# Optimization experiments

Measured on AMD Instinct MI355X. Metric: run time of the kernel, lower is better.

The kernel has to match this reference:

```python
import jax, jax.numpy as jnp
import numpy as np

B, N1, N2, D, H = 32, 512, 256, 256, 8
HD = D // H  # head dim = 32


def setup_inputs() -> dict:
    key = jax.random.key(0)
    ks = jax.random.split(key, 12)
    s = 0.05
    return {
        "x1": jax.random.normal(ks[0], (B, N1, D), jnp.float32),
        "x2": jax.random.normal(ks[1], (B, N2, D), jnp.float32),
        "r_w1": jax.random.normal(ks[2], (D, 2 * D), jnp.float32) * s,
        "r_b1": jnp.zeros((D,), jnp.float32),
        "ln_g": jnp.ones((D,), jnp.float32),
        "ln_b": jnp.zeros((D,), jnp.float32),
        "r_w2": jax.random.normal(ks[3], (4, D), jnp.float32) * s,
        "r_b2": jnp.zeros((4,), jnp.float32),
        "lf_w": jax.random.normal(ks[4], (D, D), jnp.float32) * s,
        "lf_b": jnp.zeros((D,), jnp.float32),
        "af2_w": jax.random.normal(ks[5], (D, D), jnp.float32) * s,
        "af2_b": jnp.zeros((D,), jnp.float32),
        "af3_w": jax.random.normal(ks[6], (N1, D), jnp.float32) * s,  # Linear(dim, num_pathway)
        "af3_b": jnp.zeros((N1,), jnp.float32),
        "attn_in_w": jax.random.normal(ks[7], (3 * D, D), jnp.float32) * s,
        "attn_in_b": jnp.zeros((3 * D,), jnp.float32),
        "attn_out_w": jax.random.normal(ks[8], (D, D), jnp.float32) * s,
        "attn_out_b": jnp.zeros((D,), jnp.float32),
    }


def _layernorm(x, g, b, eps=1e-5):
    mu = x.mean(-1, keepdims=True)
    var = ((x - mu) ** 2).mean(-1, keepdims=True)
    return (x - mu) * jax.lax.rsqrt(var + eps) * g + b


def reference(x1, x2, r_w1, r_b1, ln_g, ln_b, r_w2, r_b2,
              lf_w, lf_b, af2_w, af2_b, af3_w, af3_b,
              attn_in_w, attn_in_b, attn_out_w, attn_out_b):
    b, n1, d = x1.shape
    n2 = x2.shape[1]

    # ---- RoutingNetwork: mean-pool both modalities, small MLP, softmax ----
    m = jnp.concatenate([x1.mean(1), x2.mean(1)], axis=-1)        # [b, 2d]
    h = jax.nn.gelu(_layernorm(m @ r_w1.T + r_b1, ln_g, ln_b), approximate=False)
    logits = h @ r_w2.T + r_b2                                     # [b, 4]
    w = jax.nn.softmax(logits, axis=-1)                            # [b, 4]

    z = jnp.concatenate([x1, x2], axis=1)                          # [b, n1+n2, d]

    # ---- Expert 0: LinearFusion (dropout off at eval) ----
    lf = jax.nn.elu(z @ lf_w.T + lf_b)
    g0, i0 = lf[:, :n1, :], lf[:, n1:, :]

    # ---- Expert 1: AddFusion, n1 >= n2 branch (n2 == dim required) ----
    a1 = jax.nn.elu(x1 @ af2_w.T + af2_b)                          # [b, n1, d]
    a2 = jax.nn.elu(jnp.einsum('bnd,pn->bdp', x2, af3_w) + af3_b)  # [b, d, n1]
    a2 = a2.transpose(0, 2, 1)                                     # [b, n1, d]
    x_out = a1 + a2
    g1, i1 = x_out, x_out[:, :n2, :]

    # ---- Expert 2: AttentionFusion (MHA, 8 heads, self-attn over concat) ----
    qkv = z @ attn_in_w.T + attn_in_b                              # [b, S, 3d]
    q, k, v = jnp.split(qkv, 3, axis=-1)
    S = n1 + n2
    q = q.reshape(b, S, H, HD)
    k = k.reshape(b, S, H, HD)
    v = v.reshape(b, S, H, HD)
    scores = jnp.einsum('bqhd,bkhd->bhqk', q, k) / np.sqrt(HD)
    attn = jax.nn.softmax(scores, axis=-1)
    o = jnp.einsum('bhqk,bkhd->bqhd', attn, v).reshape(b, S, d)
    o = o @ attn_out_w.T + attn_out_b
    g2, i2 = o[:, :n1, :], o[:, n1:, :]

    # ---- Expert 3: IdentityFusion ----
    g3, i3 = x1, x2

    # ---- Soft-routing weighted combine ----
    gene_all = jnp.stack([g0, g1, g2, g3], axis=1)                 # [b, 4, n1, d]
    img_all = jnp.stack([i0, i1, i2, i3], axis=1)                  # [b, 4, n2, d]
    we = w[:, :, None, None]
    gene = (gene_all * we).sum(axis=1)
    img = (img_all * we).sum(axis=1)
    return gene, img
```

## Files before the change

### kernel.cpp

```cpp
#include <hip/hip_runtime.h>
#include <hip/hip_bf16.h>
#include <math.h>

#define B_ 32
#define N1_ 512
#define N2_ 256
#define D_ 256
#define S_ 768
#define IMG_OFF 4194304
#define SCALE_ 0.17677669529663689f
#define QSCALE_ (0.17677669529663689f * 1.4426950408889634f)

typedef __attribute__((ext_vector_type(8))) short bf16x8;
typedef __attribute__((ext_vector_type(4))) float f32x4;
#define MFMA16(a, b, c) __builtin_amdgcn_mfma_f32_16x16x32_bf16(a, b, c, 0, 0, 0)

__device__ __forceinline__ ushort f2b(float f) {
  __hip_bfloat16 h = __float2bfloat16(f);
  return __builtin_bit_cast(ushort, h);
}
__device__ __forceinline__ float eluf(float v) { return v > 0.f ? v : expm1f(v); }

__global__ __launch_bounds__(256) void k_prep(const float* __restrict__ x1,
                                              const float* __restrict__ x2,
                                              ushort* __restrict__ zb,
                                              float* __restrict__ mp) {
  int b = blockIdx.x >> 3, s = blockIdx.x & 7;
  int t = threadIdx.x;
  int c = t & 63;
  int rg = t >> 6;
  __shared__ float red[4][260];
  float4 s1 = {0.f, 0.f, 0.f, 0.f};
  for (int i = 0; i < 16; ++i) {
    int r = s*64 + rg*16 + i;
    float4 v = *(const float4*)(x1 + ((size_t)(b*N1_) + r)*D_ + c*4);
    s1.x += v.x; s1.y += v.y; s1.z += v.z; s1.w += v.w;
    uint2 pk;
    pk.x = (uint)f2b(v.x) | ((uint)f2b(v.y) << 16);
    pk.y = (uint)f2b(v.z) | ((uint)f2b(v.w) << 16);
    *(uint2*)(zb + (size_t)b*196608 + (size_t)r*256 + c*4) = pk;
  }
  red[rg][c*4+0] = s1.x; red[rg][c*4+1] = s1.y; red[rg][c*4+2] = s1.z; red[rg][c*4+3] = s1.w;
  __syncthreads();
  {
    float v = red[0][t] + red[1][t] + red[2][t] + red[3][t];
    mp[(size_t)(b*8+s)*512 + t] = v * (1.0f/512.0f);
  }
  __syncthreads();
  float4 s2 = {0.f, 0.f, 0.f, 0.f};
  for (int i = 0; i < 8; ++i) {
    int r = s*32 + rg*8 + i;
    float4 v = *(const float4*)(x2 + ((size_t)(b*N2_) + r)*D_ + c*4);
    s2.x += v.x; s2.y += v.y; s2.z += v.z; s2.w += v.w;
    uint2 pk;
    pk.x = (uint)f2b(v.x) | ((uint)f2b(v.y) << 16);
    pk.y = (uint)f2b(v.z) | ((uint)f2b(v.w) << 16);
    *(uint2*)(zb + (size_t)b*196608 + (size_t)(512 + r)*256 + c*4) = pk;
  }
  red[rg][c*4+0] = s2.x; red[rg][c*4+1] = s2.y; red[rg][c*4+2] = s2.z; red[rg][c*4+3] = s2.w;
  __syncthreads();
  {
    float v = red[0][t] + red[1][t] + red[2][t] + red[3][t];
    mp[(size_t)(b*8+s)*512 + 256 + t] = v * (1.0f/256.0f);
  }
}

__global__ __launch_bounds__(256) void k_wcvt(const float* __restrict__ lf_w,
                                              const float* __restrict__ af2_w,
                                              const float* __restrict__ af3_w,
                                              const float* __restrict__ attn_in_w,
                                              const float* __restrict__ attn_out_w,
                                              ushort* __restrict__ wb) {
  int g = blockIdx.x*256 + threadIdx.x;
  int e0 = g*4;
  const float* src; int loc; float sc = 1.f;
  if (e0 < 65536)       { src = lf_w;       loc = e0; }
  else if (e0 < 131072) { src = af2_w;      loc = e0 - 65536; }
  else if (e0 < 262144) { src = af3_w;      loc = e0 - 131072; }
  else if (e0 < 458752) { src = attn_in_w;  loc = e0 - 262144; if (loc < 65536) sc = QSCALE_; }
  else                  { src = attn_out_w; loc = e0 - 458752; }
  float4 v = *(const float4*)(src + loc);
  *(ushort4*)(wb + e0) = make_ushort4(f2b(v.x*sc), f2b(v.y*sc), f2b(v.z*sc), f2b(v.w*sc));
}

__global__ __launch_bounds__(256) void k_head(const float* __restrict__ mp, const float* __restrict__ r_w1,
                       const float* __restrict__ r_b1, const float* __restrict__ ln_g,
                       const float* __restrict__ ln_b, const float* __restrict__ r_w2,
                       const float* __restrict__ r_b2, float* __restrict__ wout) {
  int b = blockIdx.x;
  int j = threadIdx.x;
  __shared__ float ms[512];
  __shared__ float red[256];
  float a0 = 0.f, a1 = 0.f;
  for (int s = 0; s < 8; ++s) {
    a0 += mp[(size_t)(b*8+s)*512 + j];
    a1 += mp[(size_t)(b*8+s)*512 + 256 + j];
  }
  ms[j] = a0; ms[j+256] = a1;
  __syncthreads();
  float acc = r_b1[j];
  const float* wrow = r_w1 + (size_t)j*512;
  for (int k = 0; k < 512; ++k) acc += ms[k]*wrow[k];
  red[j] = acc; __syncthreads();
  for (int off=128; off>0; off>>=1){ if (j<off) red[j]+=red[j+off]; __syncthreads(); }
  float mu = red[0] * (1.f/256.f); __syncthreads();
  float cd = acc - mu;
  red[j] = cd*cd; __syncthreads();
  for (int off=128; off>0; off>>=1){ if (j<off) red[j]+=red[j+off]; __syncthreads(); }
  float var = red[0]*(1.f/256.f); __syncthreads();
  float xn = cd * rsqrtf(var + 1e-5f) * ln_g[j] + ln_b[j];
  float h = 0.5f*xn*(1.f+erff(xn*0.70710678118654752f));
  float lg[4];
  for (int e=0;e<4;++e){
    red[j] = h * r_w2[e*256 + j]; __syncthreads();
    for (int off=128; off>0; off>>=1){ if (j<off) red[j]+=red[j+off]; __syncthreads(); }
    lg[e] = red[0] + r_b2[e]; __syncthreads();
  }
  if (j==0){
    float mx = fmaxf(fmaxf(lg[0],lg[1]),fmaxf(lg[2],lg[3]));
    float e0=expf(lg[0]-mx),e1=expf(lg[1]-mx),e2=expf(lg[2]-mx),e3=expf(lg[3]-mx);
    float s=e0+e1+e2+e3;
    wout[b*4+0]=e0/s; wout[b*4+1]=e1/s; wout[b*4+2]=e2/s; wout[b*4+3]=e3/s;
  }
}

__global__ __launch_bounds__(256) void k_qkv(const ushort* __restrict__ zb, const ushort* __restrict__ wb,
                      const float* __restrict__ bias,
                      ushort* __restrict__ qo, ushort* __restrict__ kh,
                      ushort* __restrict__ vt) {
  int ct = blockIdx.x, nt = blockIdx.y, b = blockIdx.z;
  int tid = threadIdx.x;
  int lane = tid & 63, wid = tid >> 6;
  int wm = wid >> 1, wn = wid & 1;
  int l15 = lane & 15, quad = lane >> 4;
  __shared__ __align__(16) ushort As[128][72];
  __shared__ __align__(16) ushort Ws[128][72];
  f32x4 acc[4][4] = {};
  int n0 = nt*128, c0 = ct*128;
  int sr = tid >> 1, sc = (tid & 1) * 32;
  const ushort* arow = zb + (size_t)b*196608 + (size_t)(n0+sr)*256;
  const ushort* wrow = wb + 262144 + (size_t)(c0+sr)*256;
  for (int k0 = 0; k0 < 256; k0 += 64) {
    #pragma unroll
    for (int i = 0; i < 4; ++i) {
      *(uint4*)&As[sr][sc + 8*i] = *(const uint4*)(arow + k0 + sc + 8*i);
      *(uint4*)&Ws[sr][sc + 8*i] = *(const uint4*)(wrow + k0 + sc + 8*i);
    }
    __syncthreads();
    #pragma unroll
    for (int kc = 0; kc < 2; ++kc) {
      bf16x8 af[4], bfr[4];
      #pragma unroll
      for (int im = 0; im < 4; ++im) af[im] = *(bf16x8*)&As[wm*64 + im*16 + l15][kc*32 + quad*8];
      #pragma unroll
      for (int in = 0; in < 4; ++in) bfr[in] = *(bf16x8*)&Ws[wn*64 + in*16 + l15][kc*32 + quad*8];
      #pragma unroll
      for (int im = 0; im < 4; ++im)
        #pragma unroll
        for (int in = 0; in < 4; ++in)
          acc[im][in] = MFMA16(af[im], bfr[in], acc[im][in]);
    }
    __syncthreads();
  }
  if (ct < 2) {
    #pragma unroll
    for (int im = 0; im < 4; ++im)
      #pragma unroll
      for (int reg = 0; reg < 4; ++reg) {
        int n = n0 + wm*64 + im*16 + quad*4 + reg;
        #pragma unroll
        for (int in = 0; in < 4; ++in) {
          int c = c0 + wn*64 + in*16 + l15;
          qo[((size_t)(b*S_)+n)*256 + c] = f2b(acc[im][in][reg] + bias[c]*QSCALE_);
        }
      }
  } else if (ct < 4) {
    #pragma unroll
    for (int im = 0; im < 4; ++im)
      #pragma unroll
      for (int reg = 0; reg < 4; ++reg) {
        int n = n0 + wm*64 + im*16 + quad*4 + reg;
        #pragma unroll
        for (int in = 0; in < 4; ++in) {
          int c = c0 + wn*64 + in*16 + l15;
          int kc2 = c - 256; int h = kc2 >> 5, d = kc2 & 31;
          kh[(((size_t)(b*8+h))*S_ + n)*32 + d] = f2b(acc[im][in][reg] + bias[c]);
        }
      }
  } else {
    #pragma unroll
    for (int im = 0; im < 4; ++im) {
      int nb = n0 + wm*64 + im*16 + quad*4;
      #pragma unroll
      for (int in = 0; in < 4; ++in) {
        int c = c0 + wn*64 + in*16 + l15;
        float bs = bias[c];
        int vcol = c - 512; int h = vcol >> 5, d = vcol & 31;
        uint2 pk;
        pk.x = (uint)f2b(acc[im][in][0] + bs) | ((uint)f2b(acc[im][in][1] + bs) << 16);
        pk.y = (uint)f2b(acc[im][in][2] + bs) | ((uint)f2b(acc[im][in][3] + bs) << 16);
        *(uint2*)&vt[(((size_t)(b*8+h))*32 + d)*S_ + nb] = pk;
      }
    }
  }
}

__global__ __launch_bounds__(256) void k_attn(const ushort* __restrict__ qo,
                                              const ushort* __restrict__ kh,
                                              const ushort* __restrict__ vt,
                                              ushort* __restrict__ obuf) {
  int qhf = blockIdx.x, h = blockIdx.y, b = blockIdx.z;
  int tid = threadIdx.x;
  int lane = tid & 63, w = tid >> 6;
  int l15 = lane & 15, quad = lane >> 4;
  __shared__ __align__(16) ushort Ks[64][40];
  __shared__ __align__(16) ushort Vts[32][72];
  __shared__ __align__(16) ushort Ps[4][16][72];

  int qbase = qhf*384 + w*96;
  bf16x8 bq[6];
  #pragma unroll
  for (int u = 0; u < 6; ++u)
    bq[u] = *(const bf16x8*)(qo + ((size_t)(b*S_) + qbase + u*16 + l15)*256 + h*32 + quad*8);

  f32x4 ao[6][2] = {};
  float lacc[6] = {};

  int skr = tid >> 2, skc = (tid & 3) * 8;
  int svd = tid >> 3, svn = (tid & 7) * 8;
  const ushort* khb = kh + ((size_t)(b*8+h))*S_*32;
  const ushort* vtb = vt + ((size_t)(b*8+h))*32*S_;

  for (int kt = 0; kt < 12; ++kt) {
    __syncthreads();
    *(uint4*)&Ks[skr][skc] = *(const uint4*)(khb + (size_t)(kt*64 + skr)*32 + skc);
    *(uint4*)&Vts[svd][svn] = *(const uint4*)(vtb + (size_t)svd*S_ + kt*64 + svn);
    __syncthreads();

    bf16x8 ak[4];
    #pragma unroll
    for (int t = 0; t < 4; ++t) ak[t] = *(bf16x8*)&Ks[t*16 + l15][quad*8];
    bf16x8 av[2][2];
    #pragma unroll
    for (int im = 0; im < 2; ++im)
      #pragma unroll
      for (int kc = 0; kc < 2; ++kc)
        av[im][kc] = *(bf16x8*)&Vts[im*16 + l15][kc*32 + quad*8];

    #pragma unroll
    for (int u = 0; u < 6; ++u) {
      f32x4 sf[4];
      #pragma unroll
      for (int t = 0; t < 4; ++t) {
        f32x4 z = {0.f, 0.f, 0.f, 0.f};
        sf[t] = MFMA16(ak[t], bq[u], z);
      }
      #pragma unroll
      for (int t = 0; t < 4; ++t) {
        float p0 = __builtin_amdgcn_exp2f(sf[t][0]);
        float p1 = __builtin_amdgcn_exp2f(sf[t][1]);
        float p2 = __builtin_amdgcn_exp2f(sf[t][2]);
        float p3 = __builtin_amdgcn_exp2f(sf[t][3]);
        lacc[u] += (p0 + p1) + (p2 + p3);
        uint2 pk;
        pk.x = (uint)f2b(p0) | ((uint)f2b(p1) << 16);
        pk.y = (uint)f2b(p2) | ((uint)f2b(p3) << 16);
        *(uint2*)&Ps[w][l15][t*16 + quad*4] = pk;
      }
      #pragma unroll
      for (int kc = 0; kc < 2; ++kc) {
        bf16x8 bp = *(bf16x8*)&Ps[w][l15][kc*32 + quad*8];
        ao[u][0] = MFMA16(av[0][kc], bp, ao[u][0]);
        ao[u][1] = MFMA16(av[1][kc], bp, ao[u][1]);
      }
    }
  }
  #pragma unroll
  for (int u = 0; u < 6; ++u) {
    float l = lacc[u];
    l += __shfl_xor(l, 16, 64);
    l += __shfl_xor(l, 32, 64);
    float linv = 1.f / l;
    int n = qbase + u*16 + l15;
    ushort* orow = obuf + ((size_t)(b*S_)+n)*256 + h*32;
    #pragma unroll
    for (int im = 0; im < 2; ++im) {
      uint2 pk;
      pk.x = (uint)f2b(ao[u][im][0]*linv) | ((uint)f2b(ao[u][im][1]*linv) << 16);
      pk.y = (uint)f2b(ao[u][im][2]*linv) | ((uint)f2b(ao[u][im][3]*linv) << 16);
      *(uint2*)(orow + im*16 + quad*4) = pk;
    }
  }
}

__global__ __launch_bounds__(256) void k_out(const ushort* __restrict__ zb, const ushort* __restrict__ wb,
                      const ushort* __restrict__ ob,
                      const float* __restrict__ x1, const float* __restrict__ x2,
                      const float* __restrict__ lf_b, const float* __restrict__ af2_b,
                      const float* __restrict__ af3_b, const float* __restrict__ ao_b,
                      const float* __restrict__ wgt, float* __restrict__ out) {
  int dt = blockIdx.x, nt = blockIdx.y, b = blockIdx.z;
  int tid = threadIdx.x;
  int lane = tid & 63, wid = tid >> 6;
  int wm = wid >> 1, wn = wid & 1;
  int l15 = lane & 15, quad = lane >> 4;
  __shared__ __align__(16) ushort As[64][72];
  __shared__ __align__(16) ushort Ws[64][72];
  f32x4 a_lf[2][2] = {}, a_a1[2][2] = {}, a_a2[2][2] = {}, a_pj[2][2] = {};
  int n0 = nt*64, d0 = dt*64;
  int xr0 = ((nt < 8) ? nt : (nt - 8)) * 64;
  int sr = tid >> 2, scg = (tid & 3) * 16;

  {
    const ushort* ar = zb + (size_t)b*196608 + (size_t)(n0+sr)*256;
    const ushort* wr = wb + (size_t)(d0+sr)*256;
    for (int k0 = 0; k0 < 256; k0 += 64) {
      *(uint4*)&As[sr][scg]   = *(const uint4*)(ar + k0 + scg);
      *(uint4*)&As[sr][scg+8] = *(const uint4*)(ar + k0 + scg + 8);
      *(uint4*)&Ws[sr][scg]   = *(const uint4*)(wr + k0 + scg);
      *(uint4*)&Ws[sr][scg+8] = *(const uint4*)(wr + k0 + scg + 8);
      __syncthreads();
      #pragma unroll
      for (int kc = 0; kc < 2; ++kc) {
        bf16x8 a0 = *(bf16x8*)&As[wm*32 + l15][kc*32 + quad*8];
        bf16x8 a1 = *(bf16x8*)&As[wm*32 + 16 + l15][kc*32 + quad*8];
        bf16x8 b0 = *(bf16x8*)&Ws[wn*32 + l15][kc*32 + quad*8];
        bf16x8 b1 = *(bf16x8*)&Ws[wn*32 + 16 + l15][kc*32 + quad*8];
        a_lf[0][0] = MFMA16(a0, b0, a_lf[0][0]);
        a_lf[0][1] = MFMA16(a0, b1, a_lf[0][1]);
        a_lf[1][0] = MFMA16(a1, b0, a_lf[1][0]);
        a_lf[1][1] = MFMA16(a1, b1, a_lf[1][1]);
      }
      __syncthreads();
    }
  }
  {
    const ushort* ar = zb + (size_t)b*196608 + (size_t)(xr0+sr)*256;
    const ushort* wr = wb + 65536 + (size_t)(d0+sr)*256;
    for (int k0 = 0; k0 < 256; k0 += 64) {
      *(uint4*)&As[sr][scg]   = *(const uint4*)(ar + k0 + scg);
      *(uint4*)&As[sr][scg+8] = *(const uint4*)(ar + k0 + scg + 8);
      *(uint4*)&Ws[sr][scg]   = *(const uint4*)(wr + k0 + scg);
      *(uint4*)&Ws[sr][scg+8] = *(const uint4*)(wr + k0 + scg + 8);
      __syncthreads();
      #pragma unroll
      for (int kc = 0; kc < 2; ++kc) {
        bf16x8 a0 = *(bf16x8*)&As[wm*32 + l15][kc*32 + quad*8];
        bf16x8 a1 = *(bf16x8*)&As[wm*32 + 16 + l15][kc*32 + quad*8];
        bf16x8 b0 = *(bf16x8*)&Ws[wn*32 + l15][kc*32 + quad*8];
        bf16x8 b1 = *(bf16x8*)&Ws[wn*32 + 16 + l15][kc*32 + quad*8];
        a_a1[0][0] = MFMA16(a0, b0, a_a1[0][0]);
        a_a1[0][1] = MFMA16(a0, b1, a_a1[0][1]);
        a_a1[1][0] = MFMA16(a1, b0, a_a1[1][0]);
        a_a1[1][1] = MFMA16(a1, b1, a_a1[1][1]);
      }
      __syncthreads();
    }
  }
  {
    const ushort* ar = wb + 131072 + (size_t)(xr0+sr)*256;
    for (int k0 = 0; k0 < 256; k0 += 64) {
      *(uint4*)&As[sr][scg]   = *(const uint4*)(ar + k0 + scg);
      *(uint4*)&As[sr][scg+8] = *(const uint4*)(ar + k0 + scg + 8);
      {
        const ushort* x2r = zb + (size_t)b*196608 + (size_t)(512 + k0 + sr)*256 + d0 + scg;
        uint4 va = *(const uint4*)x2r;
        uint4 vb = *(const uint4*)(x2r + 8);
        const ushort* ea = (const ushort*)&va;
        const ushort* eb = (const ushort*)&vb;
        #pragma unroll
        for (int i = 0; i < 8; ++i) Ws[scg + i][sr] = ea[i];
        #pragma unroll
        for (int i = 0; i < 8; ++i) Ws[scg + 8 + i][sr] = eb[i];
      }
      __syncthreads();
      #pragma unroll
      for (int kc = 0; kc < 2; ++kc) {
        bf16x8 a0 = *(bf16x8*)&As[wm*32 + l15][kc*32 + quad*8];
        bf16x8 a1 = *(bf16x8*)&As[wm*32 + 16 + l15][kc*32 + quad*8];
        bf16x8 b0 = *(bf16x8*)&Ws[wn*32 + l15][kc*32 + quad*8];
        bf16x8 b1 = *(bf16x8*)&Ws[wn*32 + 16 + l15][kc*32 + quad*8];
        a_a2[0][0] = MFMA16(a0, b0, a_a2[0][0]);
        a_a2[0][1] = MFMA16(a0, b1, a_a2[0][1]);
        a_a2[1][0] = MFMA16(a1, b0, a_a2[1][0]);
        a_a2[1][1] = MFMA16(a1, b1, a_a2[1][1]);
      }
      __syncthreads();
    }
  }
  {
    const ushort* ar = ob + ((size_t)(b*S_) + n0 + sr)*256;
    const ushort* wr = wb + 458752 + (size_t)(d0+sr)*256;
    for (int k0 = 0; k0 < 256; k0 += 64) {
      *(uint4*)&As[sr][scg]   = *(const uint4*)(ar + k0 + scg);
      *(uint4*)&As[sr][scg+8] = *(const uint4*)(ar + k0 + scg + 8);
      *(uint4*)&Ws[sr][scg]   = *(const uint4*)(wr + k0 + scg);
      *(uint4*)&Ws[sr][scg+8] = *(const uint4*)(wr + k0 + scg + 8);
      __syncthreads();
      #pragma unroll
      for (int kc = 0; kc < 2; ++kc) {
        bf16x8 a0 = *(bf16x8*)&As[wm*32 + l15][kc*32 + quad*8];
        bf16x8 a1 = *(bf16x8*)&As[wm*32 + 16 + l15][kc*32 + quad*8];
        bf16x8 b0 = *(bf16x8*)&Ws[wn*32 + l15][kc*32 + quad*8];
        bf16x8 b1 = *(bf16x8*)&Ws[wn*32 + 16 + l15][kc*32 + quad*8];
        a_pj[0][0] = MFMA16(a0, b0, a_pj[0][0]);
        a_pj[0][1] = MFMA16(a0, b1, a_pj[0][1]);
        a_pj[1][0] = MFMA16(a1, b0, a_pj[1][0]);
        a_pj[1][1] = MFMA16(a1, b1, a_pj[1][1]);
      }
      __syncthreads();
    }
  }
  float w0 = wgt[b*4+0], w1v = wgt[b*4+1], w2v = wgt[b*4+2], w3 = wgt[b*4+3];
  #pragma unroll
  for (int im = 0; im < 2; ++im) {
    #pragma unroll
    for (int reg = 0; reg < 4; ++reg) {
      int rl = wm*32 + im*16 + quad*4 + reg;
      int n = n0 + rl;
      int rx = xr0 + rl;
      const float* zr; float* orw;
      if (nt < 8) { zr = x1 + ((size_t)(b*N1_) + n)*D_;      orw = out + ((size_t)(b*N1_) + n)*D_; }
      else { int j2 = n - 512; zr = x2 + ((size_t)(b*N2_) + j2)*D_;
             orw = out + (size_t)IMG_OFF + ((size_t)(b*N2_) + j2)*D_; }
      float b3 = af3_b[rx];
      #pragma unroll
      for (int in = 0; in < 2; ++in) {
        int d = d0 + wn*32 + in*16 + l15;
        float v = w0*eluf(a_lf[im][in][reg] + lf_b[d])
                + w1v*(eluf(a_a1[im][in][reg] + af2_b[d]) + eluf(a_a2[im][in][reg] + b3))
                + w2v*(a_pj[im][in][reg] + ao_b[d])
                + w3*zr[d];
        orw[d] = v;
      }
    }
  }
}

extern "C" void kernel_launch(void* const* d_in, const int* in_sizes, int n_in,
                              void* d_out, int out_size, void* d_ws, size_t ws_size,
                              hipStream_t stream) {
  const float* x1        = (const float*)d_in[0];
  const float* x2        = (const float*)d_in[1];
  const float* r_w1      = (const float*)d_in[2];
  const float* r_b1      = (const float*)d_in[3];
  const float* ln_g      = (const float*)d_in[4];
  const float* ln_b      = (const float*)d_in[5];
  const float* r_w2      = (const float*)d_in[6];
  const float* r_b2      = (const float*)d_in[7];
  const float* lf_b      = (const float*)d_in[9];
  const float* af2_b     = (const float*)d_in[11];
  const float* af3_b     = (const float*)d_in[13];
  const float* attn_in_b = (const float*)d_in[15];
  const float* attn_out_b= (const float*)d_in[17];
  float* out = (float*)d_out;

  float* ws_mp = (float*)d_ws;
  float* ws_w  = ws_mp + 131072;
  ushort* ws_zb = (ushort*)(ws_w + 128);
  ushort* ws_qo = ws_zb + (size_t)B_*S_*256;
  ushort* ws_kh = ws_qo + (size_t)B_*S_*256;
  ushort* ws_vt = ws_kh + (size_t)B_*S_*256;
  ushort* ws_wb = ws_vt + (size_t)B_*S_*256;

  k_prep<<<dim3(B_*8), 256, 0, stream>>>(x1, x2, ws_zb, ws_mp);
  k_wcvt<<<dim3(512),  256, 0, stream>>>((const float*)d_in[8], (const float*)d_in[10],
                                         (const float*)d_in[12], (const float*)d_in[14],
                                         (const float*)d_in[16], ws_wb);
  k_head<<<dim3(B_),   256, 0, stream>>>(ws_mp, r_w1, r_b1, ln_g, ln_b, r_w2, r_b2, ws_w);
  k_qkv <<<dim3(6,6,B_), 256, 0, stream>>>(ws_zb, ws_wb, attn_in_b, ws_qo, ws_kh, ws_vt);
  k_attn<<<dim3(2,8,B_), 256, 0, stream>>>(ws_qo, ws_kh, ws_vt, ws_qo);
  k_out <<<dim3(4,12,B_),256, 0, stream>>>(ws_zb, ws_wb, ws_qo, x1, x2,
                                           lf_b, af2_b, af3_b, attn_out_b, ws_w, out);
}
```

Before: 265.6 us.

## Merge weight conversion into prep kernel, fuse k_out GEMM loops, vectorize head

Folds the weight bf16 conversion kernel into the prep kernel as extra blocks, removing one launch. Restructures k_out so all four GEMMs share a single K loop with separate LDS tiles, cutting the number of barriers and letting loads for the four products overlap. The four tiles raise LDS use to about 74KB per block, which may reduce occupancy. Also vectorizes the routing-head matvec with float4 loads and adds a small packing helper.

```diff
diff --git a/kernel.cpp b/kernel.cpp
--- a/kernel.cpp
+++ b/kernel.cpp
@@ -8,7 +8,6 @@
 #define D_ 256
 #define S_ 768
 #define IMG_OFF 4194304
-#define SCALE_ 0.17677669529663689f
 #define QSCALE_ (0.17677669529663689f * 1.4426950408889634f)
 
 typedef __attribute__((ext_vector_type(8))) short bf16x8;
@@ -19,14 +18,36 @@
   __hip_bfloat16 h = __float2bfloat16(f);
   return __builtin_bit_cast(ushort, h);
 }
+__device__ __forceinline__ uint pk2(float a, float b) {
+  return (uint)f2b(a) | ((uint)f2b(b) << 16);
+}
 __device__ __forceinline__ float eluf(float v) { return v > 0.f ? v : expm1f(v); }
 
 __global__ __launch_bounds__(256) void k_prep(const float* __restrict__ x1,
                                               const float* __restrict__ x2,
+                                              const float* __restrict__ lf_w,
+                                              const float* __restrict__ af2_w,
+                                              const float* __restrict__ af3_w,
+                                              const float* __restrict__ attn_in_w,
+                                              const float* __restrict__ attn_out_w,
                                               ushort* __restrict__ zb,
+                                              ushort* __restrict__ wb,
                                               float* __restrict__ mp) {
+  int t = threadIdx.x;
+  if (blockIdx.x >= 256) {
+    int g = (blockIdx.x - 256)*256 + t;
+    int e0 = g*4;
+    const float* src; int loc; float sc = 1.f;
+    if (e0 < 65536)       { src = lf_w;       loc = e0; }
+    else if (e0 < 131072) { src = af2_w;      loc = e0 - 65536; }
+    else if (e0 < 262144) { src = af3_w;      loc = e0 - 131072; }
+    else if (e0 < 458752) { src = attn_in_w;  loc = e0 - 262144; if (loc < 65536) sc = QSCALE_; }
+    else                  { src = attn_out_w; loc = e0 - 458752; }
+    float4 v = *(const float4*)(src + loc);
+    *(ushort4*)(wb + e0) = make_ushort4(f2b(v.x*sc), f2b(v.y*sc), f2b(v.z*sc), f2b(v.w*sc));
+    return;
+  }
   int b = blockIdx.x >> 3, s = blockIdx.x & 7;
-  int t = threadIdx.x;
   int c = t & 63;
   int rg = t >> 6;
   __shared__ float red[4][260];
@@ -35,9 +56,7 @@
     int r = s*64 + rg*16 + i;
     float4 v = *(const float4*)(x1 + ((size_t)(b*N1_) + r)*D_ + c*4);
     s1.x += v.x; s1.y += v.y; s1.z += v.z; s1.w += v.w;
-    uint2 pk;
-    pk.x = (uint)f2b(v.x) | ((uint)f2b(v.y) << 16);
-    pk.y = (uint)f2b(v.z) | ((uint)f2b(v.w) << 16);
+    uint2 pk; pk.x = pk2(v.x, v.y); pk.y = pk2(v.z, v.w);
     *(uint2*)(zb + (size_t)b*196608 + (size_t)r*256 + c*4) = pk;
   }
   red[rg][c*4+0] = s1.x; red[rg][c*4+1] = s1.y; red[rg][c*4+2] = s1.z; red[rg][c*4+3] = s1.w;
@@ -52,9 +71,7 @@
     int r = s*32 + rg*8 + i;
     float4 v = *(const float4*)(x2 + ((size_t)(b*N2_) + r)*D_ + c*4);
     s2.x += v.x; s2.y += v.y; s2.z += v.z; s2.w += v.w;
-    uint2 pk;
-    pk.x = (uint)f2b(v.x) | ((uint)f2b(v.y) << 16);
-    pk.y = (uint)f2b(v.z) | ((uint)f2b(v.w) << 16);
+    uint2 pk; pk.x = pk2(v.x, v.y); pk.y = pk2(v.z, v.w);
     *(uint2*)(zb + (size_t)b*196608 + (size_t)(512 + r)*256 + c*4) = pk;
   }
   red[rg][c*4+0] = s2.x; red[rg][c*4+1] = s2.y; red[rg][c*4+2] = s2.z; red[rg][c*4+3] = s2.w;
@@ -63,24 +80,6 @@
     float v = red[0][t] + red[1][t] + red[2][t] + red[3][t];
     mp[(size_t)(b*8+s)*512 + 256 + t] = v * (1.0f/256.0f);
   }
-}
-
-__global__ __launch_bounds__(256) void k_wcvt(const float* __restrict__ lf_w,
-                                              const float* __restrict__ af2_w,
-                                              const float* __restrict__ af3_w,
-                                              const float* __restrict__ attn_in_w,
-                                              const float* __restrict__ attn_out_w,
-                                              ushort* __restrict__ wb) {
-  int g = blockIdx.x*256 + threadIdx.x;
-  int e0 = g*4;
-  const float* src; int loc; float sc = 1.f;
-  if (e0 < 65536)       { src = lf_w;       loc = e0; }
-  else if (e0 < 131072) { src = af2_w;      loc = e0 - 65536; }
-  else if (e0 < 262144) { src = af3_w;      loc = e0 - 131072; }
-  else if (e0 < 458752) { src = attn_in_w;  loc = e0 - 262144; if (loc < 65536) sc = QSCALE_; }
-  else                  { src = attn_out_w; loc = e0 - 458752; }
-  float4 v = *(const float4*)(src + loc);
-  *(ushort4*)(wb + e0) = make_ushort4(f2b(v.x*sc), f2b(v.y*sc), f2b(v.z*sc), f2b(v.w*sc));
 }
 
 __global__ __launch_bounds__(256) void k_head(const float* __restrict__ mp, const float* __restrict__ r_w1,
@@ -89,7 +88,7 @@
                        const float* __restrict__ r_b2, float* __restrict__ wout) {
   int b = blockIdx.x;
   int j = threadIdx.x;
-  __shared__ float ms[512];
+  __shared__ __align__(16) float ms[512];
   __shared__ float red[256];
   float a0 = 0.f, a1 = 0.f;
   for (int s = 0; s < 8; ++s) {
@@ -98,9 +97,14 @@
   }
   ms[j] = a0; ms[j+256] = a1;
   __syncthreads();
-  float acc = r_b1[j];
-  const float* wrow = r_w1 + (size_t)j*512;
-  for (int k = 0; k < 512; ++k) acc += ms[k]*wrow[k];
+  float4 accv = {0.f, 0.f, 0.f, 0.f};
+  const float4* wrow4 = (const float4*)(r_w1 + (size_t)j*512);
+  const float4* ms4 = (const float4*)ms;
+  for (int k = 0; k < 128; ++k) {
+    float4 w = wrow4[k], m = ms4[k];
+    accv.x += w.x*m.x; accv.y += w.y*m.y; accv.z += w.z*m.z; accv.w += w.w*m.w;
+  }
+  float acc = r_b1[j] + (accv.x + accv.y) + (accv.z + accv.w);
   red[j] = acc; __syncthreads();
   for (int off=128; off>0; off>>=1){ if (j<off) red[j]+=red[j+off]; __syncthreads(); }
   float mu = red[0] * (1.f/256.f); __syncthreads();
@@ -197,8 +201,8 @@
         float bs = bias[c];
         int vcol = c - 512; int h = vcol >> 5, d = vcol & 31;
         uint2 pk;
-        pk.x = (uint)f2b(acc[im][in][0] + bs) | ((uint)f2b(acc[im][in][1] + bs) << 16);
-        pk.y = (uint)f2b(acc[im][in][2] + bs) | ((uint)f2b(acc[im][in][3] + bs) << 16);
+        pk.x = pk2(acc[im][in][0] + bs, acc[im][in][1] + bs);
+        pk.y = pk2(acc[im][in][2] + bs, acc[im][in][3] + bs);
         *(uint2*)&vt[(((size_t)(b*8+h))*32 + d)*S_ + nb] = pk;
       }
     }
@@ -263,8 +267,8 @@
         float p3 = __builtin_amdgcn_exp2f(sf[t][3]);
         lacc[u] += (p0 + p1) + (p2 + p3);
         uint2 pk;
-        pk.x = (uint)f2b(p0) | ((uint)f2b(p1) << 16);
-        pk.y = (uint)f2b(p2) | ((uint)f2b(p3) << 16);
+        pk.x = pk2(p0, p1);
+        pk.y = pk2(p2, p3);
         *(uint2*)&Ps[w][l15][t*16 + quad*4] = pk;
       }
       #pragma unroll
@@ -286,8 +290,8 @@
     #pragma unroll
     for (int im = 0; im < 2; ++im) {
       uint2 pk;
-      pk.x = (uint)f2b(ao[u][im][0]*linv) | ((uint)f2b(ao[u][im][1]*linv) << 16);
-      pk.y = (uint)f2b(ao[u][im][2]*linv) | ((uint)f2b(ao[u][im][3]*linv) << 16);
+      pk.x = pk2(ao[u][im][0]*linv, ao[u][im][1]*linv);
+      pk.y = pk2(ao[u][im][2]*linv, ao[u][im][3]*linv);
       *(uint2*)(orow + im*16 + quad*4) = pk;
     }
   }
@@ -304,112 +308,76 @@
   int lane = tid & 63, wid = tid >> 6;
   int wm = wid >> 1, wn = wid & 1;
   int l15 = lane & 15, quad = lane >> 4;
-  __shared__ __align__(16) ushort As[64][72];
-  __shared__ __align__(16) ushort Ws[64][72];
+  __shared__ __align__(16) ushort A1[64][72];
+  __shared__ __align__(16) ushort A2[64][72];
+  __shared__ __align__(16) ushort A3[64][72];
+  __shared__ __align__(16) ushort A4[64][72];
+  __shared__ __align__(16) ushort W1s[64][72];
+  __shared__ __align__(16) ushort W2s[64][72];
+  __shared__ __align__(16) ushort W3s[64][72];
+  __shared__ __align__(16) ushort W4s[64][72];
   f32x4 a_lf[2][2] = {}, a_a1[2][2] = {}, a_a2[2][2] = {}, a_pj[2][2] = {};
   int n0 = nt*64, d0 = dt*64;
   int xr0 = ((nt < 8) ? nt : (nt - 8)) * 64;
   int sr = tid >> 2, scg = (tid & 3) * 16;
 
-  {
-    const ushort* ar = zb + (size_t)b*196608 + (size_t)(n0+sr)*256;
-    const ushort* wr = wb + (size_t)(d0+sr)*256;
-    for (int k0 = 0; k0 < 256; k0 += 64) {
-      *(uint4*)&As[sr][scg]   = *(const uint4*)(ar + k0 + scg);
-      *(uint4*)&As[sr][scg+8] = *(const uint4*)(ar + k0 + scg + 8);
-      *(uint4*)&Ws[sr][scg]   = *(const uint4*)(wr + k0 + scg);
-      *(uint4*)&Ws[sr][scg+8] = *(const uint4*)(wr + k0 + scg + 8);
-      __syncthreads();
-      #pragma unroll
-      for (int kc = 0; kc < 2; ++kc) {
-        bf16x8 a0 = *(bf16x8*)&As[wm*32 + l15][kc*32 + quad*8];
-        bf16x8 a1 = *(bf16x8*)&As[wm*32 + 16 + l15][kc*32 + quad*8];
-        bf16x8 b0 = *(bf16x8*)&Ws[wn*32 + l15][kc*32 + quad*8];
-        bf16x8 b1 = *(bf16x8*)&Ws[wn*32 + 16 + l15][kc*32 + quad*8];
-        a_lf[0][0] = MFMA16(a0, b0, a_lf[0][0]);
-        a_lf[0][1] = MFMA16(a0, b1, a_lf[0][1]);
-        a_lf[1][0] = MFMA16(a1, b0, a_lf[1][0]);
-        a_lf[1][1] = MFMA16(a1, b1, a_lf[1][1]);
-      }
-      __syncthreads();
-    }
-  }
-  {
-    const ushort* ar = zb + (size_t)b*196608 + (size_t)(xr0+sr)*256;
-    const ushort* wr = wb + 65536 + (size_t)(d0+sr)*256;
-    for (int k0 = 0; k0 < 256; k0 += 64) {
-      *(uint4*)&As[sr][scg]   = *(const uint4*)(ar + k0 + scg);
-      *(uint4*)&As[sr][scg+8] = *(const uint4*)(ar + k0 + scg + 8);
-      *(uint4*)&Ws[sr][scg]   = *(const uint4*)(wr + k0 + scg);
-      *(uint4*)&Ws[sr][scg+8] = *(const uint4*)(wr + k0 + scg + 8);
-      __syncthreads();
-      #pragma unroll
-      for (int kc = 0; kc < 2; ++kc) {
-        bf16x8 a0 = *(bf16x8*)&As[wm*32 + l15][kc*32 + quad*8];
-        bf16x8 a1 = *(bf16x8*)&As[wm*32 + 16 + l15][kc*32 + quad*8];
-        bf16x8 b0 = *(bf16x8*)&Ws[wn*32 + l15][kc*32 + quad*8];
-        bf16x8 b1 = *(bf16x8*)&Ws[wn*32 + 16 + l15][kc*32 + quad*8];
-        a_a1[0][0] = MFMA16(a0, b0, a_a1[0][0]);
-        a_a1[0][1] = MFMA16(a0, b1, a_a1[0][1]);
-        a_a1[1][0] = MFMA16(a1, b0, a_a1[1][0]);
-        a_a1[1][1] = MFMA16(a1, b1, a_a1[1][1]);
-      }
-      __syncthreads();
-    }
-  }
-  {
-    const ushort* ar = wb + 131072 + (size_t)(xr0+sr)*256;
-    for (int k0 = 0; k0 < 256; k0 += 64) {
-      *(uint4*)&As[sr][scg]   = *(const uint4*)(ar + k0 + scg);
-      *(uint4*)&As[sr][scg+8] = *(const uint4*)(ar + k0 + scg + 8);
-      {
-        const ushort* x2r = zb + (size_t)b*196608 + (size_t)(512 + k0 + sr)*256 + d0 + scg;
-        uint4 va = *(const uint4*)x2r;
-        uint4 vb = *(const uint4*)(x2r + 8);
-        const ushort* ea = (const ushort*)&va;
-        const ushort* eb = (const ushort*)&vb;
-        #pragma unroll
-        for (int i = 0; i < 8; ++i) Ws[scg + i][sr] = ea[i];
-        #pragma unroll
-        for (int i = 0; i < 8; ++i) Ws[scg + 8 + i][sr] = eb[i];
-      }
-      __syncthreads();
-      #pragma unroll
-      for (int kc = 0; kc < 2; ++kc) {
-        bf16x8 a0 = *(bf16x8*)&As[wm*32 + l15][kc*32 + quad*8];
-        bf16x8 a1 = *(bf16x8*)&As[wm*32 + 16 + l15][kc*32 + quad*8];
-        bf16x8 b0 = *(bf16x8*)&Ws[wn*32 + l15][kc*32 + quad*8];
-        bf16x8 b1 = *(bf16x8*)&Ws[wn*32 + 16 + l15][kc*32 + quad*8];
-        a_a2[0][0] = MFMA16(a0, b0, a_a2[0][0]);
-        a_a2[0][1] = MFMA16(a0, b1, a_a2[0][1]);
-        a_a2[1][0] = MFMA16(a1, b0, a_a2[1][0]);
-        a_a2[1][1] = MFMA16(a1, b1, a_a2[1][1]);
-      }
-      __syncthreads();
-    }
-  }
-  {
-    const ushort* ar = ob + ((size_t)(b*S_) + n0 + sr)*256;
-    const ushort* wr = wb + 458752 + (size_t)(d0+sr)*256;
-    for (int k0 = 0; k0 < 256; k0 += 64) {
-      *(uint4*)&As[sr][scg]   = *(const uint4*)(ar + k0 + scg);
-      *(uint4*)&As[sr][scg+8] = *(const uint4*)(ar + k0 + scg + 8);
-      *(uint4*)&Ws[sr][scg]   = *(const uint4*)(wr + k0 + scg);
-      *(uint4*)&Ws[sr][scg+8] = *(const uint4*)(wr + k0 + scg + 8);
-      __syncthreads();
-      #pragma unroll
-      for (int kc = 0; kc < 2; ++kc) {
-        bf16x8 a0 = *(bf16x8*)&As[wm*32 + l15][kc*32 + quad*8];
-        bf16x8 a1 = *(bf16x8*)&As[wm*32 + 16 + l15][kc*32 + quad*8];
-        bf16x8 b0 = *(bf16x8*)&Ws[wn*32 + l15][kc*32 + quad*8];
-        bf16x8 b1 = *(bf16x8*)&Ws[wn*32 + 16 + l15][kc*32 + quad*8];
-        a_pj[0][0] = MFMA16(a0, b0, a_pj[0][0]);
-        a_pj[0][1] = MFMA16(a0, b1, a_pj[0][1]);
-        a_pj[1][0] = MFMA16(a1, b0, a_pj[1][0]);
-        a_pj[1][1] = MFMA16(a1, b1, a_pj[1][1]);
-      }
-      __syncthreads();
-    }
+  const ushort* p_a1 = zb + (size_t)b*196608 + (size_t)(n0+sr)*256;
+  const ushort* p_a2 = zb + (size_t)b*196608 + (size_t)(xr0+sr)*256;
+  const ushort* p_a3 = wb + 131072 + (size_t)(xr0+sr)*256;
+  const ushort* p_a4 = ob + ((size_t)(b*S_) + n0 + sr)*256;
+  const ushort* p_w1 = wb + (size_t)(d0+sr)*256;
+  const ushort* p_w2 = wb + 65536 + (size_t)(d0+sr)*256;
+  const ushort* p_w4 = wb + 458752 + (size_t)(d0+sr)*256;
+
+  for (int k0 = 0; k0 < 256; k0 += 64) {
+    *(uint4*)&A1[sr][scg]    = *(const uint4*)(p_a1 + k0 + scg);
+    *(uint4*)&A1[sr][scg+8]  = *(const uint4*)(p_a1 + k0 + scg + 8);
+    *(uint4*)&A2[sr][scg]    = *(const uint4*)(p_a2 + k0 + scg);
+    *(uint4*)&A2[sr][scg+8]  = *(const uint4*)(p_a2 + k0 + scg + 8);
+    *(uint4*)&A3[sr][scg]    = *(const uint4*)(p_a3 + k0 + scg);
+    *(uint4*)&A3[sr][scg+8]  = *(const uint4*)(p_a3 + k0 + scg + 8);
+    *(uint4*)&A4[sr][scg]    = *(const uint4*)(p_a4 + k0 + scg);
+    *(uint4*)&A4[sr][scg+8]  = *(const uint4*)(p_a4 + k0 + scg + 8);
+    *(uint4*)&W1s[sr][scg]   = *(const uint4*)(p_w1 + k0 + scg);
+    *(uint4*)&W1s[sr][scg+8] = *(const uint4*)(p_w1 + k0 + scg + 8);
+    *(uint4*)&W2s[sr][scg]   = *(const uint4*)(p_w2 + k0 + scg);
+    *(uint4*)&W2s[sr][scg+8] = *(const uint4*)(p_w2 + k0 + scg + 8);
+    *(uint4*)&W4s[sr][scg]   = *(const uint4*)(p_w4 + k0 + scg);
+    *(uint4*)&W4s[sr][scg+8] = *(const uint4*)(p_w4 + k0 + scg + 8);
+    {
+      const ushort* x2r = zb + (size_t)b*196608 + (size_t)(512 + k0 + sr)*256 + d0 + scg;
+      uint4 va = *(const uint4*)x2r;
+      uint4 vb = *(const uint4*)(x2r + 8);
+      const ushort* ea = (const ushort*)&va;
+      const ushort* eb = (const ushort*)&vb;
+      #pragma unroll
+      for (int i = 0; i < 8; ++i) W3s[scg + i][sr] = ea[i];
+      #pragma unroll
+      for (int i = 0; i < 8; ++i) W3s[scg + 8 + i][sr] = eb[i];
+    }
+    __syncthreads();
+    #pragma unroll
+    for (int kc = 0; kc < 2; ++kc) {
+      int ko = kc*32 + quad*8;
+      bf16x8 x0, x1r, y0, y1;
+      x0 = *(bf16x8*)&A1[wm*32 + l15][ko];  x1r = *(bf16x8*)&A1[wm*32 + 16 + l15][ko];
+      y0 = *(bf16x8*)&W1s[wn*32 + l15][ko]; y1  = *(bf16x8*)&W1s[wn*32 + 16 + l15][ko];
+      a_lf[0][0] = MFMA16(x0, y0, a_lf[0][0]);  a_lf[0][1] = MFMA16(x0, y1, a_lf[0][1]);
+      a_lf[1][0] = MFMA16(x1r, y0, a_lf[1][0]); a_lf[1][1] = MFMA16(x1r, y1, a_lf[1][1]);
+      x0 = *(bf16x8*)&A2[wm*32 + l15][ko];  x1r = *(bf16x8*)&A2[wm*32 + 16 + l15][ko];
+      y0 = *(bf16x8*)&W2s[wn*32 + l15][ko]; y1  = *(bf16x8*)&W2s[wn*32 + 16 + l15][ko];
+      a_a1[0][0] = MFMA16(x0, y0, a_a1[0][0]);  a_a1[0][1] = MFMA16(x0, y1, a_a1[0][1]);
+      a_a1[1][0] = MFMA16(x1r, y0, a_a1[1][0]); a_a1[1][1] = MFMA16(x1r, y1, a_a1[1][1]);
+      x0 = *(bf16x8*)&A3[wm*32 + l15][ko];  x1r = *(bf16x8*)&A3[wm*32 + 16 + l15][ko];
+      y0 = *(bf16x8*)&W3s[wn*32 + l15][ko]; y1  = *(bf16x8*)&W3s[wn*32 + 16 + l15][ko];
+      a_a2[0][0] = MFMA16(x0, y0, a_a2[0][0]);  a_a2[0][1] = MFMA16(x0, y1, a_a2[0][1]);
+      a_a2[1][0] = MFMA16(x1r, y0, a_a2[1][0]); a_a2[1][1] = MFMA16(x1r, y1, a_a2[1][1]);
+      x0 = *(bf16x8*)&A4[wm*32 + l15][ko];  x1r = *(bf16x8*)&A4[wm*32 + 16 + l15][ko];
+      y0 = *(bf16x8*)&W4s[wn*32 + l15][ko]; y1  = *(bf16x8*)&W4s[wn*32 + 16 + l15][ko];
+      a_pj[0][0] = MFMA16(x0, y0, a_pj[0][0]);  a_pj[0][1] = MFMA16(x0, y1, a_pj[0][1]);
+      a_pj[1][0] = MFMA16(x1r, y0, a_pj[1][0]); a_pj[1][1] = MFMA16(x1r, y1, a_pj[1][1]);
+    }
+    __syncthreads();
   }
   float w0 = wgt[b*4+0], w1v = wgt[b*4+1], w2v = wgt[b*4+2], w3 = wgt[b*4+3];
   #pragma unroll
@@ -463,10 +431,9 @@
   ushort* ws_vt = ws_kh + (size_t)B_*S_*256;
   ushort* ws_wb = ws_vt + (size_t)B_*S_*256;
 
-  k_prep<<<dim3(B_*8), 256, 0, stream>>>(x1, x2, ws_zb, ws_mp);
-  k_wcvt<<<dim3(512),  256, 0, stream>>>((const float*)d_in[8], (const float*)d_in[10],
-                                         (const float*)d_in[12], (const float*)d_in[14],
-                                         (const float*)d_in[16], ws_wb);
+  k_prep<<<dim3(768), 256, 0, stream>>>(x1, x2, (const float*)d_in[8], (const float*)d_in[10],
+                                        (const float*)d_in[12], (const float*)d_in[14],
+                                        (const float*)d_in[16], ws_zb, ws_wb, ws_mp);
   k_head<<<dim3(B_),   256, 0, stream>>>(ws_mp, r_w1, r_b1, ln_g, ln_b, r_w2, r_b2, ws_w);
   k_qkv <<<dim3(6,6,B_), 256, 0, stream>>>(ws_zb, ws_wb, attn_in_b, ws_qo, ws_kh, ws_vt);
   k_attn<<<dim3(2,8,B_), 256, 0, stream>>>(ws_qo, ws_kh, ws_vt, ws_qo);
```

Measured after the change: 260.8 us. Within noise of the previous version (-1.8%).
